# Performance work log

Hardware: AMD Instinct MI355X
Metric: run time of the kernel (lower is better)

Reference implementation:

```python
import jax, jax.numpy as jnp
import numpy as np

D = 1024
H = 8          # MHA fallback num_heads
DH = D // H
DFF = 4096     # mlp_ratio * hidden_size
EPS = 1e-6


def _ln(x, g, b):
    mu = jnp.mean(x, axis=-1, keepdims=True)
    var = jnp.mean((x - mu) ** 2, axis=-1, keepdims=True)
    return (x - mu) * jax.lax.rsqrt(var + EPS) * g + b


def setup_inputs() -> dict:
    key = jax.random.key(0)
    ks = jax.random.split(key, 16)
    s = 0.02
    return {
        "x": jax.random.normal(ks[0], (8, 1024, D), jnp.float32),
        "c": jax.random.normal(ks[1], (8, D), jnp.float32),
        # Mamba-block (attention fallback) params
        "m_ada_w": jax.random.normal(ks[2], (D, 3 * D), jnp.float32) * s,
        "m_ada_b": jnp.zeros((3 * D,), jnp.float32),
        "m_norm_g": jnp.ones((D,), jnp.float32),
        "m_norm_b": jnp.zeros((D,), jnp.float32),
        "in_proj_w": jax.random.normal(ks[3], (3 * D, D), jnp.float32) * s,
        "in_proj_b": jnp.zeros((3 * D,), jnp.float32),
        "out_proj_w": jax.random.normal(ks[4], (D, D), jnp.float32) * s,
        "out_proj_b": jnp.zeros((D,), jnp.float32),
        # FeedForward-block params
        "f_ada_w": jax.random.normal(ks[5], (D, 3 * D), jnp.float32) * s,
        "f_ada_b": jnp.zeros((3 * D,), jnp.float32),
        "f_norm_g": jnp.ones((D,), jnp.float32),
        "f_norm_b": jnp.zeros((D,), jnp.float32),
        "w1": jax.random.normal(ks[6], (D, DFF), jnp.float32) * s,
        "b1": jnp.zeros((DFF,), jnp.float32),
        "w2": jax.random.normal(ks[7], (DFF, D), jnp.float32) * s,
        "b2": jnp.zeros((D,), jnp.float32),
    }


def reference(x, c, m_ada_w, m_ada_b, m_norm_g, m_norm_b, in_proj_w, in_proj_b,
              out_proj_w, out_proj_b, f_ada_w, f_ada_b, f_norm_g, f_norm_b,
              w1, b1, w2, b2):
    B, N, _ = x.shape
    # ---- MambaBlock (MHA fallback), dropout = identity (eval) ----
    mod = jax.nn.silu(c) @ m_ada_w + m_ada_b              # (B, 3D)
    shift, scale, gate = jnp.split(mod, 3, axis=-1)
    h = _ln(x, m_norm_g, m_norm_b)
    h = h * (1.0 + scale[:, None, :]) + shift[:, None, :]
    qkv = h @ in_proj_w.T + in_proj_b                      # (B, N, 3D)
    q, k, v = jnp.split(qkv, 3, axis=-1)
    q = q.reshape(B, N, H, DH)
    k = k.reshape(B, N, H, DH)
    v = v.reshape(B, N, H, DH)
    scores = jnp.einsum("bqhd,bkhd->bhqk", q, k) / np.sqrt(DH).astype(np.float32)
    attn = jax.nn.softmax(scores, axis=-1)
    o = jnp.einsum("bhqk,bkhd->bqhd", attn, v).reshape(B, N, D)
    o = o @ out_proj_w.T + out_proj_b
    x = x + gate[:, None, :] * o
    # ---- FeedForward block ----
    mod2 = jax.nn.silu(c) @ f_ada_w + f_ada_b
    shift2, scale2, gate2 = jnp.split(mod2, 3, axis=-1)
    h = _ln(x, f_norm_g, f_norm_b)
    h = h * (1.0 + scale2[:, None, :]) + shift2[:, None, :]
    h = jax.nn.gelu(h @ w1 + b1, approximate=False) @ w2 + b2
    return x + gate2[:, None, :] * h
```

## Files before the change

kernel.cpp:

```cpp
#include <hip/hip_runtime.h>

typedef __bf16 bf16x8 __attribute__((ext_vector_type(8)));
typedef float f32x4 __attribute__((ext_vector_type(4)));

__device__ __forceinline__ unsigned short f2bf(float f) {
    unsigned int u = __float_as_uint(f);
    unsigned int r = (u + 0x7FFFu + ((u >> 16) & 1u)) >> 16;
    return (unsigned short)r;
}

__device__ __forceinline__ void gload16(const void* g, void* l) {
    __builtin_amdgcn_global_load_lds(
        (const __attribute__((address_space(1))) unsigned int*)g,
        (__attribute__((address_space(3))) unsigned int*)l, 16, 0, 0);
}

__device__ __forceinline__ void barrier_raw() {
    asm volatile("" ::: "memory");
    __builtin_amdgcn_s_barrier();
    asm volatile("" ::: "memory");
}

__device__ __forceinline__ void vmwait0() {
    asm volatile("s_waitcnt vmcnt(0)" ::: "memory");
}

__device__ __forceinline__ float gelu_fast(float u) {
    float z = 1.595769122f * u + 0.071354816f * u * u * u;
    return u / (1.f + __expf(-z));
}

__global__ __launch_bounds__(256) void f2b4(const float* __restrict__ in,
                                            unsigned short* __restrict__ out) {
    size_t i = ((size_t)blockIdx.x * 256 + threadIdx.x) * 4;
    float4 v = *(const float4*)(in + i);
    ushort4 o;
    o.x = f2bf(v.x); o.y = f2bf(v.y); o.z = f2bf(v.z); o.w = f2bf(v.w);
    *(ushort4*)(out + i) = o;
}

__global__ __launch_bounds__(256) void transpose_f2b(const float* __restrict__ in,
                                                     unsigned short* __restrict__ out,
                                                     int R, int C) {
    __shared__ float tile[32][33];
    int r0 = blockIdx.y * 32, c0 = blockIdx.x * 32;
    int tx = threadIdx.x & 31, ty = threadIdx.x >> 5;
#pragma unroll
    for (int i = 0; i < 4; i++) {
        int r = ty + i * 8;
        tile[r][tx] = in[(size_t)(r0 + r) * C + c0 + tx];
    }
    __syncthreads();
#pragma unroll
    for (int i = 0; i < 4; i++) {
        int r = ty + i * 8;
        out[(size_t)(c0 + r) * R + r0 + tx] = f2bf(tile[tx][r]);
    }
}

__global__ __launch_bounds__(256) void transpose_v(const unsigned short* __restrict__ qkv,
                                                   unsigned short* __restrict__ vt) {
    __shared__ unsigned short tile[32][33];
    int head = blockIdx.z;
    int b = head >> 3;
    int n0 = blockIdx.x * 32, d0 = blockIdx.y * 32;
    int tx = threadIdx.x & 31, ty = threadIdx.x >> 5;
    const unsigned short* src = qkv + (size_t)(b * 1024) * 3072 + 2048 + (head & 7) * 128;
#pragma unroll
    for (int i = 0; i < 4; i++) {
        int n = ty + i * 8;
        tile[n][tx] = src[(size_t)(n0 + n) * 3072 + d0 + tx];
    }
    __syncthreads();
#pragma unroll
    for (int i = 0; i < 4; i++) {
        int d = ty + i * 8;
        vt[((size_t)head * 128 + d0 + d) * 1024 + n0 + tx] = tile[tx][d];
    }
}

__global__ __launch_bounds__(256) void ada_mod_part(const float* __restrict__ c,
                                                    const float* __restrict__ W,
                                                    float* __restrict__ partial) {
    __shared__ float sc[8 * 64];
    int kc = blockIdx.y * 64;
    for (int i = threadIdx.x; i < 512; i += 256) {
        int b = i >> 6, k = i & 63;
        float cv = c[b * 1024 + kc + k];
        sc[i] = cv / (1.f + __expf(-cv));
    }
    __syncthreads();
    int j = blockIdx.x * 256 + threadIdx.x;
    float acc[8] = {0, 0, 0, 0, 0, 0, 0, 0};
    for (int k = 0; k < 64; k++) {
        float w = W[(size_t)(kc + k) * 3072 + j];
#pragma unroll
        for (int b = 0; b < 8; b++) acc[b] += sc[b * 64 + k] * w;
    }
#pragma unroll
    for (int b = 0; b < 8; b++) partial[((size_t)blockIdx.y * 8 + b) * 3072 + j] = acc[b];
}

__global__ __launch_bounds__(256) void ada_reduce(const float* __restrict__ partial,
                                                  const float* __restrict__ bias,
                                                  float* __restrict__ out) {
    int idx = blockIdx.x * 256 + threadIdx.x;
    int b = idx / 3072;
    int jj = idx - b * 3072;
    float s = bias[jj];
#pragma unroll
    for (int ch = 0; ch < 16; ch++) s += partial[((size_t)ch * 8 + b) * 3072 + jj];
    out[idx] = s;
}

__global__ __launch_bounds__(256) void ln_mod_kernel(const float* __restrict__ x,
                                                     const float* __restrict__ gamma,
                                                     const float* __restrict__ beta,
                                                     const float* __restrict__ mods,
                                                     unsigned short* __restrict__ out) {
    int row = blockIdx.x;
    int b = row >> 10;
    float4 v = ((const float4*)(x + (size_t)row * 1024))[threadIdx.x];
    float s = v.x + v.y + v.z + v.w;
    float s2 = v.x * v.x + v.y * v.y + v.z * v.z + v.w * v.w;
#pragma unroll
    for (int d = 1; d < 64; d <<= 1) { s += __shfl_xor(s, d); s2 += __shfl_xor(s2, d); }
    __shared__ float red[8];
    int lane = threadIdx.x & 63, wid = threadIdx.x >> 6;
    if (lane == 0) { red[wid] = s; red[4 + wid] = s2; }
    __syncthreads();
    float S = red[0] + red[1] + red[2] + red[3];
    float S2 = red[4] + red[5] + red[6] + red[7];
    float mu = S * (1.f / 1024.f);
    float var = S2 * (1.f / 1024.f) - mu * mu;
    float rs = rsqrtf(var + 1e-6f);
    const float* mrow = mods + b * 3072;
    int j0 = threadIdx.x * 4;
    float hv[4] = {v.x, v.y, v.z, v.w};
    ushort4 o;
    unsigned short* op = (unsigned short*)&o;
#pragma unroll
    for (int i = 0; i < 4; i++) {
        int j = j0 + i;
        float hh = (hv[i] - mu) * rs * gamma[j] + beta[j];
        hh = hh * (1.f + mrow[1024 + j]) + mrow[j];
        op[i] = f2bf(hh);
    }
    *(ushort4*)(out + (size_t)row * 1024 + j0) = o;
}

template <int NF, int EP>
__global__ __launch_bounds__(512, 2) void gemm256(const unsigned short* __restrict__ A,
                                                  const unsigned short* __restrict__ Bt,
                                                  int N, int K, int nx,
                                                  const float* __restrict__ bias,
                                                  const float* __restrict__ xres,
                                                  const float* __restrict__ mods,
                                                  float* __restrict__ outf,
                                                  unsigned short* __restrict__ outb) {
    constexpr int BROWS = NF * 64;
    extern __shared__ __align__(16) char smem[];
    __bf16* AsB = (__bf16*)smem;
    __bf16* BsB = AsB + 2 * 256 * 64;

    int tid = threadIdx.x, lane = tid & 63, wid = tid >> 6;
    int wr = wid >> 2, wc = wid & 3;
    int t = lane & 15, g = lane >> 4;
    int xk = (t & 7) * 8;

    int nwg = gridDim.x;
    int chunk = nwg >> 3;
    int swz = (blockIdx.x & 7) * chunk + (blockIdx.x >> 3);
    int bx = swz % nx, by = swz / nx;
    int rowA0 = by * 256, colB0 = bx * BROWS;

    int rin = tid >> 3;
    int cblk = tid & 7;
    int scol = (cblk ^ (rin & 7)) * 8;

    auto stageA = [&](int nb, int half, int kt1) {
        int k0 = kt1 << 6;
        int r0 = half * 128 + rin;
        gload16(A + (size_t)(rowA0 + r0) * K + k0 + scol,
                (void*)(AsB + nb * (256 * 64) + r0 * 64 + cblk * 8));
        int r1 = r0 + 64;
        gload16(A + (size_t)(rowA0 + r1) * K + k0 + scol,
                (void*)(AsB + nb * (256 * 64) + r1 * 64 + cblk * 8));
    };
    auto stageB4 = [&](int nb, int half, int kt1) {
        int k0 = kt1 << 6;
        int r0 = half * 128 + rin;
        gload16(Bt + (size_t)(colB0 + r0) * K + k0 + scol,
                (void*)(BsB + nb * (BROWS * 64) + r0 * 64 + cblk * 8));
        int r1 = r0 + 64;
        gload16(Bt + (size_t)(colB0 + r1) * K + k0 + scol,
                (void*)(BsB + nb * (BROWS * 64) + r1 * 64 + cblk * 8));
    };
    auto stageB2 = [&](int nb, int half, int kt1) {
        int k0 = kt1 << 6;
        int r0 = half * 64 + rin;
        gload16(Bt + (size_t)(colB0 + r0) * K + k0 + scol,
                (void*)(BsB + nb * (BROWS * 64) + r0 * 64 + cblk * 8));
    };

    f32x4 acc[8][NF];
#pragma unroll
    for (int m = 0; m < 8; m++)
#pragma unroll
        for (int n = 0; n < NF; n++) acc[m][n] = (f32x4){0.f, 0.f, 0.f, 0.f};

    stageA(0, 0, 0); stageA(0, 1, 0);
    if constexpr (NF == 4) { stageB4(0, 0, 0); stageB4(0, 1, 0); }
    else                   { stageB2(0, 0, 0); stageB2(0, 1, 0); }
    vmwait0();
    barrier_raw();

    int NT = K >> 6;
#pragma unroll 1
    for (int kt = 0; kt < NT; ++kt) {
        const __bf16* Ac = AsB + (kt & 1) * (256 * 64);
        const __bf16* Bc = BsB + (kt & 1) * (BROWS * 64);
        int nb = (kt & 1) ^ 1;
        bool more = (kt + 1) < NT;

        auto LDA = [&](int m, int ks) -> bf16x8 {
            return *(const bf16x8*)(Ac + (wr * 128 + m * 16 + t) * 64 + ((ks * 32 + g * 8) ^ xk));
        };
        auto LDB = [&](int n, int ks) -> bf16x8 {
            return *(const bf16x8*)(Bc + (wc * (NF * 16) + n * 16 + t) * 64 + ((ks * 32 + g * 8) ^ xk));
        };

        if constexpr (NF == 4) {
            bf16x8 aF[4][2], bLo[2][2], bHi[2][2];
#pragma unroll
            for (int m = 0; m < 4; m++) { aF[m][0] = LDA(m, 0); aF[m][1] = LDA(m, 1); }
#pragma unroll
            for (int n = 0; n < 2; n++) { bLo[n][0] = LDB(n, 0); bLo[n][1] = LDB(n, 1); }
            if (more) stageA(nb, 0, kt + 1);
            barrier_raw();
            __builtin_amdgcn_s_setprio(1);
#pragma unroll
            for (int m = 0; m < 4; m++)
#pragma unroll
                for (int n = 0; n < 2; n++)
#pragma unroll
                    for (int ks = 0; ks < 2; ks++)
                        acc[m][n] = __builtin_amdgcn_mfma_f32_16x16x32_bf16(aF[m][ks], bLo[n][ks], acc[m][n], 0, 0, 0);
            __builtin_amdgcn_s_setprio(0);
            barrier_raw();
#pragma unroll
            for (int n = 0; n < 2; n++) { bHi[n][0] = LDB(n + 2, 0); bHi[n][1] = LDB(n + 2, 1); }
            if (more) stageA(nb, 1, kt + 1);
            barrier_raw();
            __builtin_amdgcn_s_setprio(1);
#pragma unroll
            for (int m = 0; m < 4; m++)
#pragma unroll
                for (int n = 0; n < 2; n++)
#pragma unroll
                    for (int ks = 0; ks < 2; ks++)
                        acc[m][n + 2] = __builtin_amdgcn_mfma_f32_16x16x32_bf16(aF[m][ks], bHi[n][ks], acc[m][n + 2], 0, 0, 0);
            __builtin_amdgcn_s_setprio(0);
            barrier_raw();
            bf16x8 aH[4][2];
#pragma unroll
            for (int m = 0; m < 4; m++) { aH[m][0] = LDA(m + 4, 0); aH[m][1] = LDA(m + 4, 1); }
            if (more) stageB4(nb, 0, kt + 1);
            barrier_raw();
            __builtin_amdgcn_s_setprio(1);
#pragma unroll
            for (int m = 0; m < 4; m++)
#pragma unroll
                for (int n = 0; n < 2; n++)
#pragma unroll
                    for (int ks = 0; ks < 2; ks++)
                        acc[m + 4][n + 2] = __builtin_amdgcn_mfma_f32_16x16x32_bf16(aH[m][ks], bHi[n][ks], acc[m + 4][n + 2], 0, 0, 0);
            __builtin_amdgcn_s_setprio(0);
            barrier_raw();
            if (more) stageB4(nb, 1, kt + 1);
            __builtin_amdgcn_s_setprio(1);
#pragma unroll
            for (int m = 0; m < 4; m++)
#pragma unroll
                for (int n = 0; n < 2; n++)
#pragma unroll
                    for (int ks = 0; ks < 2; ks++)
                        acc[m + 4][n] = __builtin_amdgcn_mfma_f32_16x16x32_bf16(aH[m][ks], bLo[n][ks], acc[m + 4][n], 0, 0, 0);
            __builtin_amdgcn_s_setprio(0);
            vmwait0();
            barrier_raw();
        } else {
            bf16x8 aF[4][2], bF[2][2];
#pragma unroll
            for (int m = 0; m < 4; m++) { aF[m][0] = LDA(m, 0); aF[m][1] = LDA(m, 1); }
#pragma unroll
            for (int n = 0; n < 2; n++) { bF[n][0] = LDB(n, 0); bF[n][1] = LDB(n, 1); }
            if (more) { stageA(nb, 0, kt + 1); stageB2(nb, 0, kt + 1); }
            barrier_raw();
            __builtin_amdgcn_s_setprio(1);
#pragma unroll
            for (int m = 0; m < 4; m++)
#pragma unroll
                for (int n = 0; n < 2; n++)
#pragma unroll
                    for (int ks = 0; ks < 2; ks++)
                        acc[m][n] = __builtin_amdgcn_mfma_f32_16x16x32_bf16(aF[m][ks], bF[n][ks], acc[m][n], 0, 0, 0);
            __builtin_amdgcn_s_setprio(0);
            barrier_raw();
            bf16x8 aH[4][2];
#pragma unroll
            for (int m = 0; m < 4; m++) { aH[m][0] = LDA(m + 4, 0); aH[m][1] = LDA(m + 4, 1); }
            if (more) { stageA(nb, 1, kt + 1); stageB2(nb, 1, kt + 1); }
            barrier_raw();
            __builtin_amdgcn_s_setprio(1);
#pragma unroll
            for (int m = 0; m < 4; m++)
#pragma unroll
                for (int n = 0; n < 2; n++)
#pragma unroll
                    for (int ks = 0; ks < 2; ks++)
                        acc[m + 4][n] = __builtin_amdgcn_mfma_f32_16x16x32_bf16(aH[m][ks], bF[n][ks], acc[m + 4][n], 0, 0, 0);
            __builtin_amdgcn_s_setprio(0);
            vmwait0();
            barrier_raw();
        }
    }

    int row0 = rowA0 + wr * 128, col0 = colB0 + wc * (NF * 16);
#pragma unroll
    for (int m = 0; m < 8; m++)
#pragma unroll
        for (int n = 0; n < NF; n++) {
            int col = col0 + n * 16 + t;
#pragma unroll
            for (int r = 0; r < 4; r++) {
                int row = row0 + m * 16 + g * 4 + r;
                float v = acc[m][n][r];
                if (EP == 0) {
                    outb[(size_t)row * N + col] = f2bf(v + bias[col]);
                } else if (EP == 1) {
                    int bb = row >> 10;
                    float gt = mods[bb * 3072 + 2048 + col];
                    outf[(size_t)row * 1024 + col] =
                        xres[(size_t)row * 1024 + col] + gt * (v + bias[col]);
                } else if (EP == 2) {
                    outb[(size_t)row * N + col] = f2bf(gelu_fast(v + bias[col]));
                } else {
                    int bb = row >> 10;
                    float gt = mods[bb * 3072 + 2048 + col];
                    outf[(size_t)row * 1024 + col] += gt * (v + bias[col]);
                }
            }
        }
}

__global__ __launch_bounds__(512, 4) void attn_kernel(const unsigned short* __restrict__ qkv,
                                                      const unsigned short* __restrict__ vt,
                                                      unsigned short* __restrict__ o) {
    extern __shared__ __align__(16) char asmem[];
    __bf16* Ks = (__bf16*)asmem;
    __bf16* Vts = Ks + 2 * 64 * 128;

    int bid = blockIdx.x;
    int logical = (bid & 7) * 64 + (bid >> 3);
    int q0 = (logical & 7) * 128;
    int bh = logical >> 3;
    int b = bh >> 3, h = bh & 7;
    int tid = threadIdx.x, lane = tid & 63, w = tid >> 6;
    int t = lane & 15, g = lane >> 4;
    int swzt = (t & 7) << 4;

    const unsigned short* qbase = qkv + (size_t)(b * 1024) * 3072 + h * 128;
    int qrow = q0 + w * 16 + t;
    bf16x8 qf[4];
#pragma unroll
    for (int ks = 0; ks < 4; ks++)
        qf[ks] = *(const bf16x8*)(qbase + (size_t)qrow * 3072 + ks * 32 + g * 8);

    f32x4 Oa[8];
#pragma unroll
    for (int n = 0; n < 8; n++) Oa[n] = (f32x4){0.f, 0.f, 0.f, 0.f};
    float m_r = -1e30f, l_r = 0.f;
    const float scale = 0.08838834764831845f;

    int krow = tid >> 4;
    int ksrc = (((tid & 15) * 16) ^ ((krow & 7) << 4)) >> 1;
    int vrow = tid >> 3;
    int vsrc = (((tid & 7) * 16) ^ ((vrow & 7) << 4)) >> 1;
    const unsigned short* vtg = vt + (size_t)bh * 128 * 1024;

    auto stage = [&](int buf, int kv0) {
        const unsigned short* kb = qkv + (size_t)(b * 1024 + kv0) * 3072 + 1024 + h * 128;
#pragma unroll
        for (int cc = 0; cc < 2; cc++) {
            gload16(kb + (size_t)(cc * 32 + krow) * 3072 + ksrc,
                    (void*)(Ks + buf * 8192 + cc * 4096 + tid * 8));
            gload16(vtg + (size_t)(cc * 64 + vrow) * 1024 + kv0 + vsrc,
                    (void*)(Vts + buf * 8192 + cc * 4096 + tid * 8));
        }
    };

    stage(0, 0);
    vmwait0();
    barrier_raw();

#pragma unroll 1
    for (int tile = 0; tile < 16; ++tile) {
        int cur = tile & 1;
        bool more = tile < 15;
        if (more) stage(cur ^ 1, (tile + 1) * 64);
        const __bf16* Kc = Ks + cur * 8192;
        const __bf16* Vc = Vts + cur * 8192;

        f32x4 St[4];
#pragma unroll
        for (int n = 0; n < 4; n++) St[n] = (f32x4){0.f, 0.f, 0.f, 0.f};
        __builtin_amdgcn_s_setprio(1);
#pragma unroll
        for (int ks = 0; ks < 4; ks++) {
#pragma unroll
            for (int n = 0; n < 4; n++) {
                bf16x8 kf = *(const bf16x8*)&Kc[(n * 16 + t) * 128 + (((ks * 64 + g * 16) ^ swzt) >> 1)];
                St[n] = __builtin_amdgcn_mfma_f32_16x16x32_bf16(kf, qf[ks], St[n], 0, 0, 0);
            }
        }
        __builtin_amdgcn_s_setprio(0);

        float mx = -1e30f;
#pragma unroll
        for (int n = 0; n < 4; n++)
#pragma unroll
            for (int r = 0; r < 4; r++) mx = fmaxf(mx, St[n][r]);
        mx *= scale;
        mx = fmaxf(mx, __shfl_xor(mx, 16));
        mx = fmaxf(mx, __shfl_xor(mx, 32));
        float mn = fmaxf(m_r, mx);
        float alpha = __expf(m_r - mn);
        m_r = mn;
        float p[4][4];
        float rs = 0.f;
#pragma unroll
        for (int n = 0; n < 4; n++)
#pragma unroll
            for (int r = 0; r < 4; r++) {
                float pv = __expf(St[n][r] * scale - mn);
                p[n][r] = pv;
                rs += pv;
            }
        rs += __shfl_xor(rs, 16);
        rs += __shfl_xor(rs, 32);
        l_r = l_r * alpha + rs;

        unsigned P01[4], P23[4];
#pragma unroll
        for (int n = 0; n < 4; n++) {
            P01[n] = (unsigned)f2bf(p[n][0]) | ((unsigned)f2bf(p[n][1]) << 16);
            P23[n] = (unsigned)f2bf(p[n][2]) | ((unsigned)f2bf(p[n][3]) << 16);
        }

#pragma unroll
        for (int r = 0; r < 4; r++) {
            float ar = __shfl(alpha, (lane & 48) + g * 4 + r);
#pragma unroll
            for (int n2 = 0; n2 < 8; n2++) Oa[n2][r] *= ar;
        }

#pragma unroll
        for (int ks2 = 0; ks2 < 2; ks2++) {
            int e = ks2 * 2, od = ks2 * 2 + 1;
            unsigned s16a = (g < 2) ? P01[e] : P01[od];
            unsigned s16b = (g < 2) ? P23[e] : P23[od];
            unsigned s32a = (g & 1) ? P01[e] : P01[od];
            unsigned s32b = (g & 1) ? P23[e] : P23[od];
            unsigned s48a = (g >= 2) ? P01[e] : P01[od];
            unsigned s48b = (g >= 2) ? P23[e] : P23[od];
            unsigned r16a = __shfl_xor(s16a, 16), r16b = __shfl_xor(s16b, 16);
            unsigned r32a = __shfl_xor(s32a, 32), r32b = __shfl_xor(s32b, 32);
            unsigned r48a = __shfl_xor(s48a, 48), r48b = __shfl_xor(s48b, 48);
            union { unsigned u[4]; bf16x8 v; } pa;
            pa.u[0] = (g == 0) ? P01[e] : (g == 1) ? r48a : (g == 2) ? r32a : r16a;
            pa.u[1] = (g == 0) ? P23[e] : (g == 1) ? r48b : (g == 2) ? r32b : r16b;
            pa.u[2] = (g == 0) ? r16a : (g == 1) ? r32a : (g == 2) ? r48a : P01[od];
            pa.u[3] = (g == 0) ? r16b : (g == 1) ? r32b : (g == 2) ? r48b : P23[od];
            __builtin_amdgcn_s_setprio(1);
#pragma unroll
            for (int n2 = 0; n2 < 8; n2++) {
                bf16x8 vf = *(const bf16x8*)&Vc[(n2 * 16 + t) * 64 + (((ks2 * 64 + g * 16) ^ swzt) >> 1)];
                Oa[n2] = __builtin_amdgcn_mfma_f32_16x16x32_bf16(pa.v, vf, Oa[n2], 0, 0, 0);
            }
            __builtin_amdgcn_s_setprio(0);
        }

        if (more) { vmwait0(); barrier_raw(); }
    }

#pragma unroll
    for (int r = 0; r < 4; r++) {
        float lq = __shfl(l_r, (lane & 48) + g * 4 + r);
        float inv = 1.f / lq;
        int orow = q0 + w * 16 + g * 4 + r;
#pragma unroll
        for (int n2 = 0; n2 < 8; n2++)
            o[(size_t)(b * 1024 + orow) * 1024 + h * 128 + n2 * 16 + t] = f2bf(Oa[n2][r] * inv);
    }
}

extern "C" void kernel_launch(void* const* d_in, const int* in_sizes, int n_in,
                              void* d_out, int out_size, void* d_ws, size_t ws_size,
                              hipStream_t stream) {
    const float* x          = (const float*)d_in[0];
    const float* c          = (const float*)d_in[1];
    const float* m_ada_w    = (const float*)d_in[2];
    const float* m_ada_b    = (const float*)d_in[3];
    const float* m_norm_g   = (const float*)d_in[4];
    const float* m_norm_b   = (const float*)d_in[5];
    const float* in_proj_w  = (const float*)d_in[6];
    const float* in_proj_b  = (const float*)d_in[7];
    const float* out_proj_w = (const float*)d_in[8];
    const float* out_proj_b = (const float*)d_in[9];
    const float* f_ada_w    = (const float*)d_in[10];
    const float* f_ada_b    = (const float*)d_in[11];
    const float* f_norm_g   = (const float*)d_in[12];
    const float* f_norm_b   = (const float*)d_in[13];
    const float* w1         = (const float*)d_in[14];
    const float* b1         = (const float*)d_in[15];
    const float* w2         = (const float*)d_in[16];
    const float* b2         = (const float*)d_in[17];
    float* out = (float*)d_out;
    char* ws = (char*)d_ws;

    unsigned short* Wq   = (unsigned short*)(ws + 0);
    unsigned short* Wo   = (unsigned short*)(ws + 6291456);
    unsigned short* vt   = (unsigned short*)(ws + 8388608);
    unsigned short* W1t  = (unsigned short*)(ws + 8388608);
    unsigned short* W2t  = (unsigned short*)(ws + 16777216);
    float*          modm = (float*)(ws + 25165824);
    float*          modf = (float*)(ws + 25264128);
    unsigned short* hbuf = (unsigned short*)(ws + 25362432);
    float*          part = (float*)(ws + 25362432);
    float*          part2= (float*)(ws + 25362432 + 2097152);
    unsigned short* qkv  = (unsigned short*)(ws + 42139648);
    unsigned short* obuf = (unsigned short*)(ws + 92471296);
    unsigned short* h2   = (unsigned short*)(ws + 42139648);

    hipFuncSetAttribute((const void*)&gemm256<4, 0>, hipFuncAttributeMaxDynamicSharedMemorySize, 131072);
    hipFuncSetAttribute((const void*)&gemm256<4, 2>, hipFuncAttributeMaxDynamicSharedMemorySize, 131072);
    hipFuncSetAttribute((const void*)&gemm256<2, 1>, hipFuncAttributeMaxDynamicSharedMemorySize, 98304);
    hipFuncSetAttribute((const void*)&gemm256<2, 3>, hipFuncAttributeMaxDynamicSharedMemorySize, 98304);
    hipFuncSetAttribute((const void*)&attn_kernel, hipFuncAttributeMaxDynamicSharedMemorySize, 65536);

    hipLaunchKernelGGL(ada_mod_part, dim3(12, 16), dim3(256), 0, stream, c, m_ada_w, part);
    hipLaunchKernelGGL(ada_mod_part, dim3(12, 16), dim3(256), 0, stream, c, f_ada_w, part2);
    hipLaunchKernelGGL(ada_reduce, dim3(96), dim3(256), 0, stream, part, m_ada_b, modm);
    hipLaunchKernelGGL(ada_reduce, dim3(96), dim3(256), 0, stream, part2, f_ada_b, modf);

    hipLaunchKernelGGL(f2b4, dim3(3072), dim3(256), 0, stream, in_proj_w, Wq);
    hipLaunchKernelGGL(f2b4, dim3(1024), dim3(256), 0, stream, out_proj_w, Wo);

    hipLaunchKernelGGL(ln_mod_kernel, dim3(8192), dim3(256), 0, stream, x, m_norm_g, m_norm_b, modm, hbuf);
    hipLaunchKernelGGL(HIP_KERNEL_NAME(gemm256<4, 0>), dim3(384), dim3(512), 131072, stream,
                       hbuf, Wq, 3072, 1024, 12, in_proj_b, (const float*)nullptr,
                       (const float*)nullptr, (float*)nullptr, qkv);
    hipLaunchKernelGGL(transpose_v, dim3(32, 4, 64), dim3(256), 0, stream, qkv, vt);
    hipLaunchKernelGGL(attn_kernel, dim3(512), dim3(512), 65536, stream, qkv, vt, obuf);
    hipLaunchKernelGGL(HIP_KERNEL_NAME(gemm256<2, 1>), dim3(256), dim3(512), 98304, stream,
                       obuf, Wo, 1024, 1024, 8, out_proj_b, x, modm, out, (unsigned short*)nullptr);

    hipLaunchKernelGGL(transpose_f2b, dim3(128, 32), dim3(256), 0, stream, w1, W1t, 1024, 4096);
    hipLaunchKernelGGL(transpose_f2b, dim3(32, 128), dim3(256), 0, stream, w2, W2t, 4096, 1024);

    hipLaunchKernelGGL(ln_mod_kernel, dim3(8192), dim3(256), 0, stream, out, f_norm_g, f_norm_b, modf, hbuf);
    hipLaunchKernelGGL(HIP_KERNEL_NAME(gemm256<4, 2>), dim3(512), dim3(512), 131072, stream,
                       hbuf, W1t, 4096, 1024, 16, b1, (const float*)nullptr,
                       (const float*)nullptr, (float*)nullptr, h2);
    hipLaunchKernelGGL(HIP_KERNEL_NAME(gemm256<2, 3>), dim3(256), dim3(512), 98304, stream,
                       h2, W2t, 1024, 4096, 8, b2, (const float*)nullptr, modf, out,
                       (unsigned short*)nullptr);
}
```

Before: 392.7 us.

## Replace ping-pong GEMM with simpler BK=32 double-buffered templated kernel

Rewrites the bf16 MFMA GEMM as a generic template over wave layout. It uses a 32-wide K tile, an unswizzled LDS layout, and a single stage-then-compute loop with one barrier per k-step. LDS use per block is halved, which may allow more blocks per CU. The change drops the XOR swizzle and the interleaved partial-tile scheduling, which risks LDS bank conflicts and more barrier overhead per unit of work.

```diff
diff --git a/kernel.cpp b/kernel.cpp
--- a/kernel.cpp
+++ b/kernel.cpp
@@ -149,188 +149,91 @@
     *(ushort4*)(out + (size_t)row * 1024 + j0) = o;
 }
 
-template <int NF, int EP>
-__global__ __launch_bounds__(512, 2) void gemm256(const unsigned short* __restrict__ A,
-                                                  const unsigned short* __restrict__ Bt,
-                                                  int N, int K, int nx,
-                                                  const float* __restrict__ bias,
-                                                  const float* __restrict__ xres,
-                                                  const float* __restrict__ mods,
-                                                  float* __restrict__ outf,
-                                                  unsigned short* __restrict__ outb) {
+template <int NF, int WR, int WC, int EP>
+__global__ __launch_bounds__(512) void gemmk(const unsigned short* __restrict__ A,
+                                             const unsigned short* __restrict__ Bt,
+                                             int N, int K, int nx,
+                                             const float* __restrict__ bias,
+                                             const float* __restrict__ xres,
+                                             const float* __restrict__ mods,
+                                             float* __restrict__ outf,
+                                             unsigned short* __restrict__ outb) {
     constexpr int BROWS = NF * 64;
+    constexpr int MR = 256 / (16 * WR);
+    constexpr int NR = BROWS / (16 * WC);
+    constexpr int AE = 256 * 32;
+    constexpr int BE = BROWS * 32;
     extern __shared__ __align__(16) char smem[];
-    __bf16* AsB = (__bf16*)smem;
-    __bf16* BsB = AsB + 2 * 256 * 64;
+    __bf16* As = (__bf16*)smem;
+    __bf16* Bs = As + 2 * AE;
 
     int tid = threadIdx.x, lane = tid & 63, wid = tid >> 6;
-    int wr = wid >> 2, wc = wid & 3;
+    int wr = wid / WC, wc = wid % WC;
     int t = lane & 15, g = lane >> 4;
-    int xk = (t & 7) * 8;
-
-    int nwg = gridDim.x;
-    int chunk = nwg >> 3;
+
+    int nwg = gridDim.x, chunk = nwg >> 3;
     int swz = (blockIdx.x & 7) * chunk + (blockIdx.x >> 3);
     int bx = swz % nx, by = swz / nx;
     int rowA0 = by * 256, colB0 = bx * BROWS;
 
-    int rin = tid >> 3;
-    int cblk = tid & 7;
-    int scol = (cblk ^ (rin & 7)) * 8;
-
-    auto stageA = [&](int nb, int half, int kt1) {
-        int k0 = kt1 << 6;
-        int r0 = half * 128 + rin;
-        gload16(A + (size_t)(rowA0 + r0) * K + k0 + scol,
-                (void*)(AsB + nb * (256 * 64) + r0 * 64 + cblk * 8));
-        int r1 = r0 + 64;
-        gload16(A + (size_t)(rowA0 + r1) * K + k0 + scol,
-                (void*)(AsB + nb * (256 * 64) + r1 * 64 + cblk * 8));
+    int rin = tid >> 2, cq = (tid & 3) * 8;
+
+    auto stage = [&](int nb, int kt1) {
+        int k0 = kt1 << 5;
+        gload16(A + (size_t)(rowA0 + rin) * K + k0 + cq, (void*)(As + nb * AE + tid * 8));
+        gload16(A + (size_t)(rowA0 + 128 + rin) * K + k0 + cq,
+                (void*)(As + nb * AE + 4096 + tid * 8));
+        gload16(Bt + (size_t)(colB0 + rin) * K + k0 + cq, (void*)(Bs + nb * BE + tid * 8));
+        if constexpr (NF == 4)
+            gload16(Bt + (size_t)(colB0 + 128 + rin) * K + k0 + cq,
+                    (void*)(Bs + nb * BE + 4096 + tid * 8));
     };
-    auto stageB4 = [&](int nb, int half, int kt1) {
-        int k0 = kt1 << 6;
-        int r0 = half * 128 + rin;
-        gload16(Bt + (size_t)(colB0 + r0) * K + k0 + scol,
-                (void*)(BsB + nb * (BROWS * 64) + r0 * 64 + cblk * 8));
-        int r1 = r0 + 64;
-        gload16(Bt + (size_t)(colB0 + r1) * K + k0 + scol,
-                (void*)(BsB + nb * (BROWS * 64) + r1 * 64 + cblk * 8));
-    };
-    auto stageB2 = [&](int nb, int half, int kt1) {
-        int k0 = kt1 << 6;
-        int r0 = half * 64 + rin;
-        gload16(Bt + (size_t)(colB0 + r0) * K + k0 + scol,
-                (void*)(BsB + nb * (BROWS * 64) + r0 * 64 + cblk * 8));
-    };
-
-    f32x4 acc[8][NF];
-#pragma unroll
-    for (int m = 0; m < 8; m++)
-#pragma unroll
-        for (int n = 0; n < NF; n++) acc[m][n] = (f32x4){0.f, 0.f, 0.f, 0.f};
-
-    stageA(0, 0, 0); stageA(0, 1, 0);
-    if constexpr (NF == 4) { stageB4(0, 0, 0); stageB4(0, 1, 0); }
-    else                   { stageB2(0, 0, 0); stageB2(0, 1, 0); }
+
+    f32x4 acc[MR][NR];
+#pragma unroll
+    for (int m = 0; m < MR; m++)
+#pragma unroll
+        for (int n = 0; n < NR; n++) acc[m][n] = (f32x4){0.f, 0.f, 0.f, 0.f};
+
+    stage(0, 0);
     vmwait0();
     barrier_raw();
 
-    int NT = K >> 6;
+    int NT = K >> 5;
 #pragma unroll 1
     for (int kt = 0; kt < NT; ++kt) {
-        const __bf16* Ac = AsB + (kt & 1) * (256 * 64);
-        const __bf16* Bc = BsB + (kt & 1) * (BROWS * 64);
-        int nb = (kt & 1) ^ 1;
+        const __bf16* Ac = As + (kt & 1) * AE;
+        const __bf16* Bc = Bs + (kt & 1) * BE;
         bool more = (kt + 1) < NT;
-
-        auto LDA = [&](int m, int ks) -> bf16x8 {
-            return *(const bf16x8*)(Ac + (wr * 128 + m * 16 + t) * 64 + ((ks * 32 + g * 8) ^ xk));
-        };
-        auto LDB = [&](int n, int ks) -> bf16x8 {
-            return *(const bf16x8*)(Bc + (wc * (NF * 16) + n * 16 + t) * 64 + ((ks * 32 + g * 8) ^ xk));
-        };
-
-        if constexpr (NF == 4) {
-            bf16x8 aF[4][2], bLo[2][2], bHi[2][2];
-#pragma unroll
-            for (int m = 0; m < 4; m++) { aF[m][0] = LDA(m, 0); aF[m][1] = LDA(m, 1); }
-#pragma unroll
-            for (int n = 0; n < 2; n++) { bLo[n][0] = LDB(n, 0); bLo[n][1] = LDB(n, 1); }
-            if (more) stageA(nb, 0, kt + 1);
-            barrier_raw();
-            __builtin_amdgcn_s_setprio(1);
-#pragma unroll
-            for (int m = 0; m < 4; m++)
-#pragma unroll
-                for (int n = 0; n < 2; n++)
-#pragma unroll
-                    for (int ks = 0; ks < 2; ks++)
-                        acc[m][n] = __builtin_amdgcn_mfma_f32_16x16x32_bf16(aF[m][ks], bLo[n][ks], acc[m][n], 0, 0, 0);
-            __builtin_amdgcn_s_setprio(0);
-            barrier_raw();
-#pragma unroll
-            for (int n = 0; n < 2; n++) { bHi[n][0] = LDB(n + 2, 0); bHi[n][1] = LDB(n + 2, 1); }
-            if (more) stageA(nb, 1, kt + 1);
-            barrier_raw();
-            __builtin_amdgcn_s_setprio(1);
-#pragma unroll
-            for (int m = 0; m < 4; m++)
-#pragma unroll
-                for (int n = 0; n < 2; n++)
-#pragma unroll
-                    for (int ks = 0; ks < 2; ks++)
-                        acc[m][n + 2] = __builtin_amdgcn_mfma_f32_16x16x32_bf16(aF[m][ks], bHi[n][ks], acc[m][n + 2], 0, 0, 0);
-            __builtin_amdgcn_s_setprio(0);
-            barrier_raw();
-            bf16x8 aH[4][2];
-#pragma unroll
-            for (int m = 0; m < 4; m++) { aH[m][0] = LDA(m + 4, 0); aH[m][1] = LDA(m + 4, 1); }
-            if (more) stageB4(nb, 0, kt + 1);
-            barrier_raw();
-            __builtin_amdgcn_s_setprio(1);
-#pragma unroll
-            for (int m = 0; m < 4; m++)
-#pragma unroll
-                for (int n = 0; n < 2; n++)
-#pragma unroll
-                    for (int ks = 0; ks < 2; ks++)
-                        acc[m + 4][n + 2] = __builtin_amdgcn_mfma_f32_16x16x32_bf16(aH[m][ks], bHi[n][ks], acc[m + 4][n + 2], 0, 0, 0);
-            __builtin_amdgcn_s_setprio(0);
-            barrier_raw();
-            if (more) stageB4(nb, 1, kt + 1);
-            __builtin_amdgcn_s_setprio(1);
-#pragma unroll
-            for (int m = 0; m < 4; m++)
-#pragma unroll
-                for (int n = 0; n < 2; n++)
-#pragma unroll
-                    for (int ks = 0; ks < 2; ks++)
-                        acc[m + 4][n] = __builtin_amdgcn_mfma_f32_16x16x32_bf16(aH[m][ks], bLo[n][ks], acc[m + 4][n], 0, 0, 0);
-            __builtin_amdgcn_s_setprio(0);
+        if (more) stage((kt & 1) ^ 1, kt + 1);
+
+        bf16x8 a[MR], b[NR];
+#pragma unroll
+        for (int m = 0; m < MR; m++)
+            a[m] = *(const bf16x8*)&Ac[(wr * (MR * 16) + m * 16 + t) * 32 + g * 8];
+#pragma unroll
+        for (int n = 0; n < NR; n++)
+            b[n] = *(const bf16x8*)&Bc[(wc * (NR * 16) + n * 16 + t) * 32 + g * 8];
+
+        __builtin_amdgcn_s_setprio(1);
+#pragma unroll
+        for (int m = 0; m < MR; m++)
+#pragma unroll
+            for (int n = 0; n < NR; n++)
+                acc[m][n] = __builtin_amdgcn_mfma_f32_16x16x32_bf16(a[m], b[n], acc[m][n], 0, 0, 0);
+        __builtin_amdgcn_s_setprio(0);
+
+        if (more) {
             vmwait0();
             barrier_raw();
-        } else {
-            bf16x8 aF[4][2], bF[2][2];
-#pragma unroll
-            for (int m = 0; m < 4; m++) { aF[m][0] = LDA(m, 0); aF[m][1] = LDA(m, 1); }
-#pragma unroll
-            for (int n = 0; n < 2; n++) { bF[n][0] = LDB(n, 0); bF[n][1] = LDB(n, 1); }
-            if (more) { stageA(nb, 0, kt + 1); stageB2(nb, 0, kt + 1); }
-            barrier_raw();
-            __builtin_amdgcn_s_setprio(1);
-#pragma unroll
-            for (int m = 0; m < 4; m++)
-#pragma unroll
-                for (int n = 0; n < 2; n++)
-#pragma unroll
-                    for (int ks = 0; ks < 2; ks++)
-                        acc[m][n] = __builtin_amdgcn_mfma_f32_16x16x32_bf16(aF[m][ks], bF[n][ks], acc[m][n], 0, 0, 0);
-            __builtin_amdgcn_s_setprio(0);
-            barrier_raw();
-            bf16x8 aH[4][2];
-#pragma unroll
-            for (int m = 0; m < 4; m++) { aH[m][0] = LDA(m + 4, 0); aH[m][1] = LDA(m + 4, 1); }
-            if (more) { stageA(nb, 1, kt + 1); stageB2(nb, 1, kt + 1); }
-            barrier_raw();
-            __builtin_amdgcn_s_setprio(1);
-#pragma unroll
-            for (int m = 0; m < 4; m++)
-#pragma unroll
-                for (int n = 0; n < 2; n++)
-#pragma unroll
-                    for (int ks = 0; ks < 2; ks++)
-                        acc[m + 4][n] = __builtin_amdgcn_mfma_f32_16x16x32_bf16(aH[m][ks], bF[n][ks], acc[m + 4][n], 0, 0, 0);
-            __builtin_amdgcn_s_setprio(0);
-            vmwait0();
-            barrier_raw();
-        }
-    }
-
-    int row0 = rowA0 + wr * 128, col0 = colB0 + wc * (NF * 16);
-#pragma unroll
-    for (int m = 0; m < 8; m++)
-#pragma unroll
-        for (int n = 0; n < NF; n++) {
+        }
+    }
+
+    int row0 = rowA0 + wr * (MR * 16), col0 = colB0 + wc * (NR * 16);
+#pragma unroll
+    for (int m = 0; m < MR; m++)
+#pragma unroll
+        for (int n = 0; n < NR; n++) {
             int col = col0 + n * 16 + t;
 #pragma unroll
             for (int r = 0; r < 4; r++) {
@@ -543,10 +446,10 @@
     unsigned short* obuf = (unsigned short*)(ws + 92471296);
     unsigned short* h2   = (unsigned short*)(ws + 42139648);
 
-    hipFuncSetAttribute((const void*)&gemm256<4, 0>, hipFuncAttributeMaxDynamicSharedMemorySize, 131072);
-    hipFuncSetAttribute((const void*)&gemm256<4, 2>, hipFuncAttributeMaxDynamicSharedMemorySize, 131072);
-    hipFuncSetAttribute((const void*)&gemm256<2, 1>, hipFuncAttributeMaxDynamicSharedMemorySize, 98304);
-    hipFuncSetAttribute((const void*)&gemm256<2, 3>, hipFuncAttributeMaxDynamicSharedMemorySize, 98304);
+    hipFuncSetAttribute((const void*)&gemmk<4, 2, 4, 0>, hipFuncAttributeMaxDynamicSharedMemorySize, 65536);
+    hipFuncSetAttribute((const void*)&gemmk<4, 2, 4, 2>, hipFuncAttributeMaxDynamicSharedMemorySize, 65536);
+    hipFuncSetAttribute((const void*)&gemmk<2, 4, 2, 1>, hipFuncAttributeMaxDynamicSharedMemorySize, 49152);
+    hipFuncSetAttribute((const void*)&gemmk<2, 4, 2, 3>, hipFuncAttributeMaxDynamicSharedMemorySize, 49152);
     hipFuncSetAttribute((const void*)&attn_kernel, hipFuncAttributeMaxDynamicSharedMemorySize, 65536);
 
     hipLaunchKernelGGL(ada_mod_part, dim3(12, 16), dim3(256), 0, stream, c, m_ada_w, part);
@@ -558,22 +461,22 @@
     hipLaunchKernelGGL(f2b4, dim3(1024), dim3(256), 0, stream, out_proj_w, Wo);
 
     hipLaunchKernelGGL(ln_mod_kernel, dim3(8192), dim3(256), 0, stream, x, m_norm_g, m_norm_b, modm, hbuf);
-    hipLaunchKernelGGL(HIP_KERNEL_NAME(gemm256<4, 0>), dim3(384), dim3(512), 131072, stream,
+    hipLaunchKernelGGL(HIP_KERNEL_NAME(gemmk<4, 2, 4, 0>), dim3(384), dim3(512), 65536, stream,
                        hbuf, Wq, 3072, 1024, 12, in_proj_b, (const float*)nullptr,
                        (const float*)nullptr, (float*)nullptr, qkv);
     hipLaunchKernelGGL(transpose_v, dim3(32, 4, 64), dim3(256), 0, stream, qkv, vt);
     hipLaunchKernelGGL(attn_kernel, dim3(512), dim3(512), 65536, stream, qkv, vt, obuf);
-    hipLaunchKernelGGL(HIP_KERNEL_NAME(gemm256<2, 1>), dim3(256), dim3(512), 98304, stream,
+    hipLaunchKernelGGL(HIP_KERNEL_NAME(gemmk<2, 4, 2, 1>), dim3(256), dim3(512), 49152, stream,
                        obuf, Wo, 1024, 1024, 8, out_proj_b, x, modm, out, (unsigned short*)nullptr);
 
     hipLaunchKernelGGL(transpose_f2b, dim3(128, 32), dim3(256), 0, stream, w1, W1t, 1024, 4096);
     hipLaunchKernelGGL(transpose_f2b, dim3(32, 128), dim3(256), 0, stream, w2, W2t, 4096, 1024);
 
     hipLaunchKernelGGL(ln_mod_kernel, dim3(8192), dim3(256), 0, stream, out, f_norm_g, f_norm_b, modf, hbuf);
-    hipLaunchKernelGGL(HIP_KERNEL_NAME(gemm256<4, 2>), dim3(512), dim3(512), 131072, stream,
+    hipLaunchKernelGGL(HIP_KERNEL_NAME(gemmk<4, 2, 4, 2>), dim3(512), dim3(512), 65536, stream,
                        hbuf, W1t, 4096, 1024, 16, b1, (const float*)nullptr,
                        (const float*)nullptr, (float*)nullptr, h2);
-    hipLaunchKernelGGL(HIP_KERNEL_NAME(gemm256<2, 3>), dim3(256), dim3(512), 98304, stream,
+    hipLaunchKernelGGL(HIP_KERNEL_NAME(gemmk<2, 4, 2, 3>), dim3(256), dim3(512), 49152, stream,
                        h2, W2t, 1024, 4096, 8, b2, (const float*)nullptr, modf, out,
                        (unsigned short*)nullptr);
 }
```

Result: slower. 404.3 us (+2.9%).

## Restructure GEMM mainloop into deeper prefetch pipeline with split half-tiles

Applied to the files above, without the earlier changes.

Rewrites the shared GEMM kernel so LDS holds A and B as separately addressed halves, and global-to-LDS loads are issued two k-tiles ahead instead of one. Partial vmcnt waits replace full drains, so loads stay in flight across iterations. The NF=2 and NF=4 variants are unified into one four-phase MFMA schedule with explicit lgkmcnt fences. This aims to hide global memory latency better in all four GEMMs, at the cost of tighter wait-count correctness and more complex buffer reuse.

```diff
diff --git a/kernel.cpp b/kernel.cpp
--- a/kernel.cpp
+++ b/kernel.cpp
@@ -21,8 +21,9 @@
     asm volatile("" ::: "memory");
 }
 
-__device__ __forceinline__ void vmwait0() {
-    asm volatile("s_waitcnt vmcnt(0)" ::: "memory");
+__device__ __forceinline__ void lgkm0_fence() {
+    asm volatile("s_waitcnt lgkmcnt(0)" ::: "memory");
+    __builtin_amdgcn_sched_barrier(0);
 }
 
 __device__ __forceinline__ float gelu_fast(float u) {
@@ -150,58 +151,55 @@
 }
 
 template <int NF, int EP>
-__global__ __launch_bounds__(512, 2) void gemm256(const unsigned short* __restrict__ A,
-                                                  const unsigned short* __restrict__ Bt,
-                                                  int N, int K, int nx,
-                                                  const float* __restrict__ bias,
-                                                  const float* __restrict__ xres,
-                                                  const float* __restrict__ mods,
-                                                  float* __restrict__ outf,
-                                                  unsigned short* __restrict__ outb) {
-    constexpr int BROWS = NF * 64;
+__global__ __launch_bounds__(512, 2) void gemm8p(const unsigned short* __restrict__ A,
+                                                 const unsigned short* __restrict__ Bt,
+                                                 int N, int K, int nx,
+                                                 const float* __restrict__ bias,
+                                                 const float* __restrict__ xres,
+                                                 const float* __restrict__ mods,
+                                                 float* __restrict__ outf,
+                                                 unsigned short* __restrict__ outb) {
+    constexpr int BN = NF * 64;
+    constexpr int NH = NF / 2;
+    constexpr int HA = 8192;
+    constexpr int HB = NF * 2048;
+    constexpr int CIF = (NF == 4) ? 6 : 5;
     extern __shared__ __align__(16) char smem[];
-    __bf16* AsB = (__bf16*)smem;
-    __bf16* BsB = AsB + 2 * 256 * 64;
+    __bf16* As = (__bf16*)smem;
+    __bf16* Bs = As + 4 * HA;
 
     int tid = threadIdx.x, lane = tid & 63, wid = tid >> 6;
     int wr = wid >> 2, wc = wid & 3;
     int t = lane & 15, g = lane >> 4;
     int xk = (t & 7) * 8;
 
-    int nwg = gridDim.x;
-    int chunk = nwg >> 3;
+    int nwg = gridDim.x, chunk = nwg >> 3;
     int swz = (blockIdx.x & 7) * chunk + (blockIdx.x >> 3);
     int bx = swz % nx, by = swz / nx;
-    int rowA0 = by * 256, colB0 = bx * BROWS;
-
-    int rin = tid >> 3;
-    int cblk = tid & 7;
+    int rowA0 = by * 256, colB0 = bx * BN;
+
+    int rin = tid >> 3, cblk = tid & 7;
     int scol = (cblk ^ (rin & 7)) * 8;
 
-    auto stageA = [&](int nb, int half, int kt1) {
-        int k0 = kt1 << 6;
-        int r0 = half * 128 + rin;
-        gload16(A + (size_t)(rowA0 + r0) * K + k0 + scol,
-                (void*)(AsB + nb * (256 * 64) + r0 * 64 + cblk * 8));
-        int r1 = r0 + 64;
-        gload16(A + (size_t)(rowA0 + r1) * K + k0 + scol,
-                (void*)(AsB + nb * (256 * 64) + r1 * 64 + cblk * 8));
+    auto stageAh = [&](int d, int h, int kt) {
+        int k0 = kt << 6;
+        const unsigned short* src = A + (size_t)(rowA0 + h * 128 + rin) * K + k0 + scol;
+        __bf16* dst = As + (d * 2 + h) * HA + tid * 8;
+        gload16(src, dst);
+        gload16(src + (size_t)64 * K, dst + 4096);
     };
-    auto stageB4 = [&](int nb, int half, int kt1) {
-        int k0 = kt1 << 6;
-        int r0 = half * 128 + rin;
-        gload16(Bt + (size_t)(colB0 + r0) * K + k0 + scol,
-                (void*)(BsB + nb * (BROWS * 64) + r0 * 64 + cblk * 8));
-        int r1 = r0 + 64;
-        gload16(Bt + (size_t)(colB0 + r1) * K + k0 + scol,
-                (void*)(BsB + nb * (BROWS * 64) + r1 * 64 + cblk * 8));
+    auto stageBh = [&](int d, int h, int kt) {
+        int k0 = kt << 6;
+        if constexpr (NF == 4) {
+            const unsigned short* src = Bt + (size_t)(colB0 + h * 128 + rin) * K + k0 + scol;
+            __bf16* dst = Bs + (d * 2 + h) * HB + tid * 8;
+            gload16(src, dst);
+            gload16(src + (size_t)64 * K, dst + 4096);
+        } else {
+            const unsigned short* src = Bt + (size_t)(colB0 + h * 64 + rin) * K + k0 + scol;
+            gload16(src, Bs + (d * 2 + h) * HB + tid * 8);
+        }
     };
-    auto stageB2 = [&](int nb, int half, int kt1) {
-        int k0 = kt1 << 6;
-        int r0 = half * 64 + rin;
-        gload16(Bt + (size_t)(colB0 + r0) * K + k0 + scol,
-                (void*)(BsB + nb * (BROWS * 64) + r0 * 64 + cblk * 8));
-    };
 
     f32x4 acc[8][NF];
 #pragma unroll
@@ -209,119 +207,94 @@
 #pragma unroll
         for (int n = 0; n < NF; n++) acc[m][n] = (f32x4){0.f, 0.f, 0.f, 0.f};
 
-    stageA(0, 0, 0); stageA(0, 1, 0);
-    if constexpr (NF == 4) { stageB4(0, 0, 0); stageB4(0, 1, 0); }
-    else                   { stageB2(0, 0, 0); stageB2(0, 1, 0); }
-    vmwait0();
+    int NT = K >> 6;
+    stageAh(0, 0, 0); stageAh(0, 1, 0); stageBh(0, 0, 0); stageBh(0, 1, 0);
+    stageAh(1, 0, 1); stageAh(1, 1, 1); stageBh(1, 0, 1);
+    asm volatile("s_waitcnt vmcnt(%0)" :: "i"(CIF) : "memory");
     barrier_raw();
 
-    int NT = K >> 6;
 #pragma unroll 1
     for (int kt = 0; kt < NT; ++kt) {
-        const __bf16* Ac = AsB + (kt & 1) * (256 * 64);
-        const __bf16* Bc = BsB + (kt & 1) * (BROWS * 64);
-        int nb = (kt & 1) ^ 1;
-        bool more = (kt + 1) < NT;
+        int d = kt & 1, dn = d ^ 1;
+        const __bf16* Ab = As + (d * 2 + wr) * HA;
+        const __bf16* Bb = Bs + (d * 2 + (wc >> 1)) * HB;
+        bool s1 = kt + 1 < NT, s2 = kt + 2 < NT;
 
         auto LDA = [&](int m, int ks) -> bf16x8 {
-            return *(const bf16x8*)(Ac + (wr * 128 + m * 16 + t) * 64 + ((ks * 32 + g * 8) ^ xk));
+            return *(const bf16x8*)&Ab[(m * 16 + t) * 64 + ((ks * 32 + g * 8) ^ xk)];
         };
         auto LDB = [&](int n, int ks) -> bf16x8 {
-            return *(const bf16x8*)(Bc + (wc * (NF * 16) + n * 16 + t) * 64 + ((ks * 32 + g * 8) ^ xk));
+            int row = (NF == 4 ? (wc & 1) * 64 : (wc & 1) * 32) + n * 16 + t;
+            return *(const bf16x8*)&Bb[row * 64 + ((ks * 32 + g * 8) ^ xk)];
         };
 
-        if constexpr (NF == 4) {
-            bf16x8 aF[4][2], bLo[2][2], bHi[2][2];
-#pragma unroll
-            for (int m = 0; m < 4; m++) { aF[m][0] = LDA(m, 0); aF[m][1] = LDA(m, 1); }
-#pragma unroll
-            for (int n = 0; n < 2; n++) { bLo[n][0] = LDB(n, 0); bLo[n][1] = LDB(n, 1); }
-            if (more) stageA(nb, 0, kt + 1);
-            barrier_raw();
-            __builtin_amdgcn_s_setprio(1);
-#pragma unroll
-            for (int m = 0; m < 4; m++)
-#pragma unroll
-                for (int n = 0; n < 2; n++)
-#pragma unroll
-                    for (int ks = 0; ks < 2; ks++)
-                        acc[m][n] = __builtin_amdgcn_mfma_f32_16x16x32_bf16(aF[m][ks], bLo[n][ks], acc[m][n], 0, 0, 0);
-            __builtin_amdgcn_s_setprio(0);
-            barrier_raw();
-#pragma unroll
-            for (int n = 0; n < 2; n++) { bHi[n][0] = LDB(n + 2, 0); bHi[n][1] = LDB(n + 2, 1); }
-            if (more) stageA(nb, 1, kt + 1);
-            barrier_raw();
-            __builtin_amdgcn_s_setprio(1);
-#pragma unroll
-            for (int m = 0; m < 4; m++)
-#pragma unroll
-                for (int n = 0; n < 2; n++)
-#pragma unroll
-                    for (int ks = 0; ks < 2; ks++)
-                        acc[m][n + 2] = __builtin_amdgcn_mfma_f32_16x16x32_bf16(aF[m][ks], bHi[n][ks], acc[m][n + 2], 0, 0, 0);
-            __builtin_amdgcn_s_setprio(0);
-            barrier_raw();
-            bf16x8 aH[4][2];
-#pragma unroll
-            for (int m = 0; m < 4; m++) { aH[m][0] = LDA(m + 4, 0); aH[m][1] = LDA(m + 4, 1); }
-            if (more) stageB4(nb, 0, kt + 1);
-            barrier_raw();
-            __builtin_amdgcn_s_setprio(1);
-#pragma unroll
-            for (int m = 0; m < 4; m++)
-#pragma unroll
-                for (int n = 0; n < 2; n++)
-#pragma unroll
-                    for (int ks = 0; ks < 2; ks++)
-                        acc[m + 4][n + 2] = __builtin_amdgcn_mfma_f32_16x16x32_bf16(aH[m][ks], bHi[n][ks], acc[m + 4][n + 2], 0, 0, 0);
-            __builtin_amdgcn_s_setprio(0);
-            barrier_raw();
-            if (more) stageB4(nb, 1, kt + 1);
-            __builtin_amdgcn_s_setprio(1);
-#pragma unroll
-            for (int m = 0; m < 4; m++)
-#pragma unroll
-                for (int n = 0; n < 2; n++)
-#pragma unroll
-                    for (int ks = 0; ks < 2; ks++)
-                        acc[m + 4][n] = __builtin_amdgcn_mfma_f32_16x16x32_bf16(aH[m][ks], bLo[n][ks], acc[m + 4][n], 0, 0, 0);
-            __builtin_amdgcn_s_setprio(0);
-            vmwait0();
-            barrier_raw();
-        } else {
-            bf16x8 aF[4][2], bF[2][2];
-#pragma unroll
-            for (int m = 0; m < 4; m++) { aF[m][0] = LDA(m, 0); aF[m][1] = LDA(m, 1); }
-#pragma unroll
-            for (int n = 0; n < 2; n++) { bF[n][0] = LDB(n, 0); bF[n][1] = LDB(n, 1); }
-            if (more) { stageA(nb, 0, kt + 1); stageB2(nb, 0, kt + 1); }
-            barrier_raw();
-            __builtin_amdgcn_s_setprio(1);
-#pragma unroll
-            for (int m = 0; m < 4; m++)
-#pragma unroll
-                for (int n = 0; n < 2; n++)
-#pragma unroll
-                    for (int ks = 0; ks < 2; ks++)
-                        acc[m][n] = __builtin_amdgcn_mfma_f32_16x16x32_bf16(aF[m][ks], bF[n][ks], acc[m][n], 0, 0, 0);
-            __builtin_amdgcn_s_setprio(0);
-            barrier_raw();
-            bf16x8 aH[4][2];
-#pragma unroll
-            for (int m = 0; m < 4; m++) { aH[m][0] = LDA(m + 4, 0); aH[m][1] = LDA(m + 4, 1); }
-            if (more) { stageA(nb, 1, kt + 1); stageB2(nb, 1, kt + 1); }
-            barrier_raw();
-            __builtin_amdgcn_s_setprio(1);
-#pragma unroll
-            for (int m = 0; m < 4; m++)
-#pragma unroll
-                for (int n = 0; n < 2; n++)
-#pragma unroll
-                    for (int ks = 0; ks < 2; ks++)
-                        acc[m + 4][n] = __builtin_amdgcn_mfma_f32_16x16x32_bf16(aH[m][ks], bF[n][ks], acc[m + 4][n], 0, 0, 0);
-            __builtin_amdgcn_s_setprio(0);
-            vmwait0();
+        bf16x8 aF[4][2], aH[4][2], bL[NH][2], bH[NH][2];
+
+#pragma unroll
+        for (int m = 0; m < 4; m++) { aF[m][0] = LDA(m, 0); aF[m][1] = LDA(m, 1); }
+#pragma unroll
+        for (int n = 0; n < NH; n++) { bL[n][0] = LDB(n, 0); bL[n][1] = LDB(n, 1); }
+        if (s1) stageBh(dn, 1, kt + 1);
+        barrier_raw();
+        lgkm0_fence();
+        __builtin_amdgcn_s_setprio(1);
+#pragma unroll
+        for (int m = 0; m < 4; m++)
+#pragma unroll
+            for (int n = 0; n < NH; n++)
+#pragma unroll
+                for (int ks = 0; ks < 2; ks++)
+                    acc[m][n] = __builtin_amdgcn_mfma_f32_16x16x32_bf16(aF[m][ks], bL[n][ks], acc[m][n], 0, 0, 0);
+        __builtin_amdgcn_s_setprio(0);
+        barrier_raw();
+
+#pragma unroll
+        for (int m = 0; m < 4; m++) { aH[m][0] = LDA(m + 4, 0); aH[m][1] = LDA(m + 4, 1); }
+        barrier_raw();
+        lgkm0_fence();
+        __builtin_amdgcn_s_setprio(1);
+#pragma unroll
+        for (int m = 0; m < 4; m++)
+#pragma unroll
+            for (int n = 0; n < NH; n++)
+#pragma unroll
+                for (int ks = 0; ks < 2; ks++)
+                    acc[m + 4][n] = __builtin_amdgcn_mfma_f32_16x16x32_bf16(aH[m][ks], bL[n][ks], acc[m + 4][n], 0, 0, 0);
+        __builtin_amdgcn_s_setprio(0);
+        barrier_raw();
+
+#pragma unroll
+        for (int n = 0; n < NH; n++) { bH[n][0] = LDB(n + NH, 0); bH[n][1] = LDB(n + NH, 1); }
+        if (s2) stageAh(d, 0, kt + 2);
+        barrier_raw();
+        lgkm0_fence();
+        __builtin_amdgcn_s_setprio(1);
+#pragma unroll
+        for (int m = 0; m < 4; m++)
+#pragma unroll
+            for (int n = 0; n < NH; n++)
+#pragma unroll
+                for (int ks = 0; ks < 2; ks++)
+                    acc[m][n + NH] = __builtin_amdgcn_mfma_f32_16x16x32_bf16(aF[m][ks], bH[n][ks], acc[m][n + NH], 0, 0, 0);
+        __builtin_amdgcn_s_setprio(0);
+        barrier_raw();
+
+        if (s2) { stageAh(d, 1, kt + 2); stageBh(d, 0, kt + 2); }
+        __builtin_amdgcn_s_setprio(1);
+#pragma unroll
+        for (int m = 0; m < 4; m++)
+#pragma unroll
+            for (int n = 0; n < NH; n++)
+#pragma unroll
+                for (int ks = 0; ks < 2; ks++)
+                    acc[m + 4][n + NH] = __builtin_amdgcn_mfma_f32_16x16x32_bf16(aH[m][ks], bH[n][ks], acc[m + 4][n + NH], 0, 0, 0);
+        __builtin_amdgcn_s_setprio(0);
+        if (s1) {
+            if (s2) {
+                asm volatile("s_waitcnt vmcnt(%0)" :: "i"(CIF) : "memory");
+            } else {
+                asm volatile("s_waitcnt vmcnt(0)" ::: "memory");
+            }
             barrier_raw();
         }
     }
@@ -401,7 +374,7 @@
     };
 
     stage(0, 0);
-    vmwait0();
+    asm volatile("s_waitcnt vmcnt(0)" ::: "memory");
     barrier_raw();
 
 #pragma unroll 1
@@ -491,7 +464,10 @@
             __builtin_amdgcn_s_setprio(0);
         }
 
-        if (more) { vmwait0(); barrier_raw(); }
+        if (more) {
+            asm volatile("s_waitcnt vmcnt(0)" ::: "memory");
+            barrier_raw();
+        }
     }
 
 #pragma unroll
@@ -543,10 +519,10 @@
     unsigned short* obuf = (unsigned short*)(ws + 92471296);
     unsigned short* h2   = (unsigned short*)(ws + 42139648);
 
-    hipFuncSetAttribute((const void*)&gemm256<4, 0>, hipFuncAttributeMaxDynamicSharedMemorySize, 131072);
-    hipFuncSetAttribute((const void*)&gemm256<4, 2>, hipFuncAttributeMaxDynamicSharedMemorySize, 131072);
-    hipFuncSetAttribute((const void*)&gemm256<2, 1>, hipFuncAttributeMaxDynamicSharedMemorySize, 98304);
-    hipFuncSetAttribute((const void*)&gemm256<2, 3>, hipFuncAttributeMaxDynamicSharedMemorySize, 98304);
+    hipFuncSetAttribute((const void*)&gemm8p<4, 0>, hipFuncAttributeMaxDynamicSharedMemorySize, 131072);
+    hipFuncSetAttribute((const void*)&gemm8p<4, 2>, hipFuncAttributeMaxDynamicSharedMemorySize, 131072);
+    hipFuncSetAttribute((const void*)&gemm8p<2, 1>, hipFuncAttributeMaxDynamicSharedMemorySize, 98304);
+    hipFuncSetAttribute((const void*)&gemm8p<2, 3>, hipFuncAttributeMaxDynamicSharedMemorySize, 98304);
     hipFuncSetAttribute((const void*)&attn_kernel, hipFuncAttributeMaxDynamicSharedMemorySize, 65536);
 
     hipLaunchKernelGGL(ada_mod_part, dim3(12, 16), dim3(256), 0, stream, c, m_ada_w, part);
@@ -558,22 +534,22 @@
     hipLaunchKernelGGL(f2b4, dim3(1024), dim3(256), 0, stream, out_proj_w, Wo);
 
     hipLaunchKernelGGL(ln_mod_kernel, dim3(8192), dim3(256), 0, stream, x, m_norm_g, m_norm_b, modm, hbuf);
-    hipLaunchKernelGGL(HIP_KERNEL_NAME(gemm256<4, 0>), dim3(384), dim3(512), 131072, stream,
+    hipLaunchKernelGGL(HIP_KERNEL_NAME(gemm8p<4, 0>), dim3(384), dim3(512), 131072, stream,
                        hbuf, Wq, 3072, 1024, 12, in_proj_b, (const float*)nullptr,
                        (const float*)nullptr, (float*)nullptr, qkv);
     hipLaunchKernelGGL(transpose_v, dim3(32, 4, 64), dim3(256), 0, stream, qkv, vt);
     hipLaunchKernelGGL(attn_kernel, dim3(512), dim3(512), 65536, stream, qkv, vt, obuf);
-    hipLaunchKernelGGL(HIP_KERNEL_NAME(gemm256<2, 1>), dim3(256), dim3(512), 98304, stream,
+    hipLaunchKernelGGL(HIP_KERNEL_NAME(gemm8p<2, 1>), dim3(256), dim3(512), 98304, stream,
                        obuf, Wo, 1024, 1024, 8, out_proj_b, x, modm, out, (unsigned short*)nullptr);
 
     hipLaunchKernelGGL(transpose_f2b, dim3(128, 32), dim3(256), 0, stream, w1, W1t, 1024, 4096);
     hipLaunchKernelGGL(transpose_f2b, dim3(32, 128), dim3(256), 0, stream, w2, W2t, 4096, 1024);
 
     hipLaunchKernelGGL(ln_mod_kernel, dim3(8192), dim3(256), 0, stream, out, f_norm_g, f_norm_b, modf, hbuf);
-    hipLaunchKernelGGL(HIP_KERNEL_NAME(gemm256<4, 2>), dim3(512), dim3(512), 131072, stream,
+    hipLaunchKernelGGL(HIP_KERNEL_NAME(gemm8p<4, 2>), dim3(512), dim3(512), 131072, stream,
                        hbuf, W1t, 4096, 1024, 16, b1, (const float*)nullptr,
                        (const float*)nullptr, (float*)nullptr, h2);
-    hipLaunchKernelGGL(HIP_KERNEL_NAME(gemm256<2, 3>), dim3(256), dim3(512), 98304, stream,
+    hipLaunchKernelGGL(HIP_KERNEL_NAME(gemm8p<2, 3>), dim3(256), dim3(512), 98304, stream,
                        h2, W2t, 1024, 4096, 8, b2, (const float*)nullptr, modf, out,
                        (unsigned short*)nullptr);
 }
```

Result: faster. 384.5 us (-2.1%).
